# Kernel optimization log

Hardware: AMD Instinct MI355X
Metric: run time of the kernel (lower is better)

## Reference

```python
import jax, jax.numpy as jnp
import numpy as np

N_NODES = 100000
N_EDGES = 1600000
IN_FEATS = 256
DIMS = [IN_FEATS, 128, 64, 16, 40]


def setup_inputs() -> dict:
    key = jax.random.key(0)
    ks = jax.random.split(key, 3 + 2 * 4)
    x = jax.random.normal(ks[0], (N_NODES, IN_FEATS), dtype=jnp.float32)
    src = jax.random.randint(ks[1], (N_EDGES,), 0, N_NODES)
    dst = jax.random.randint(ks[2], (N_EDGES,), 0, N_NODES)
    inp = {"x": x, "src": src, "dst": dst}
    for i in range(4):
        fan_in = DIMS[i]
        inp[f"W{i+1}"] = jax.random.normal(ks[3 + 2 * i], (DIMS[i], DIMS[i + 1]), dtype=jnp.float32) / np.sqrt(fan_in)
        inp[f"b{i+1}"] = jnp.zeros((DIMS[i + 1],), dtype=jnp.float32)
    return inp


def reference(x, src, dst, W1, b1, W2, b2, W3, b3, W4, b4):
    n = x.shape[0]
    ones = jnp.ones(src.shape[0], dtype=x.dtype)
    # symmetric GCN normalization (DGL norm='both'); clamp deg>=1 like DGL
    deg_out = jnp.maximum(jax.ops.segment_sum(ones, src, num_segments=n), 1.0)
    deg_in = jnp.maximum(jax.ops.segment_sum(ones, dst, num_segments=n), 1.0)
    norm_src = jax.lax.rsqrt(deg_out)[:, None]  # [N,1]
    norm_dst = jax.lax.rsqrt(deg_in)[:, None]   # [N,1]

    def gconv(h, W, b, act):
        # project first (in_feats >= out_feats for every layer, matching DGL ordering)
        h = (h * norm_src) @ W                                   # [N, d_out]
        h = jax.ops.segment_sum(h[src], dst, num_segments=n)      # SpMM aggregate
        h = h * norm_dst + b
        return jax.nn.relu(h) if act else h

    h = gconv(x, W1, b1, True)
    h = gconv(h, W2, b2, True)
    h = gconv(h, W3, b3, True)
    h = gconv(h, W4, b4, False)
    return h
```

## Files before the change

kernel.cpp:

```cpp
#include <hip/hip_runtime.h>


typedef unsigned short ushort_t;
#define CAP 64

__device__ __forceinline__ void gload_lds16(const float4* g, float4* l) {
    __builtin_amdgcn_global_load_lds(
        (const __attribute__((address_space(1))) void*)g,
        (__attribute__((address_space(3))) void*)l, 16, 0, 0);
}

__device__ __forceinline__ ushort_t f2bf(float f) {
    unsigned u = __float_as_uint(f);
    u += 0x7FFFu + ((u >> 16) & 1u);
    return (ushort_t)(u >> 16);
}
__device__ __forceinline__ unsigned pack2bf(float a, float b) {
    return (unsigned)f2bf(a) | ((unsigned)f2bf(b) << 16);
}
__device__ __forceinline__ float nrm_of(int d) {
    return rsqrtf((float)(d > 1 ? d : 1));
}
#define BFLO(u) __uint_as_float((u) << 16)
#define BFHI(u) __uint_as_float((u) & 0xffff0000u)

template<int DIN, int DOUT, int RB, int KT, typename EPI>
__device__ __forceinline__ void proj_body(
        const float* __restrict__ in, const float* __restrict__ W,
        int N, int n0, float4* __restrict__ wlds, float4* __restrict__ xlds,
        EPI&& epi) {
    constexpr int CG  = DOUT / 4;
    constexpr int RPP = 256 / CG;
    constexpr int R4  = RB / RPP;
    constexpr int K4T = KT / 4;
    constexpr int NKT = DIN / KT;
    constexpr int XTILE = RB * K4T;
    constexpr int WTILE = KT * CG;

    const int tid  = threadIdx.x;
    const int wave = tid >> 6;
    const int lane = tid & 63;
    const int rp   = tid / CG;
    const int cg   = tid - rp * CG;

    float4 acc[R4];
#pragma unroll
    for (int r = 0; r < R4; ++r) acc[r] = make_float4(0.f, 0.f, 0.f, 0.f);

    for (int kt = 0; kt < NKT; ++kt) {
        const float4* wsrc = (const float4*)(W + (size_t)kt * KT * DOUT);
#pragma unroll
        for (int j = 0; j < WTILE / 256; ++j) {
            int base = j * 256 + wave * 64;
            gload_lds16(wsrc + base + lane, &wlds[base]);
        }
#pragma unroll
        for (int j = 0; j < XTILE / 256; ++j) {
            int base = j * 256 + wave * 64;
            int fi   = base + lane;
            int row  = fi / K4T;
            int k4   = fi - row * K4T;
            int k4s  = k4 ^ (row & (K4T - 1));
            int grow = n0 + row; if (grow >= N) grow = N - 1;
            const float4* gsrc = (const float4*)(in + (size_t)grow * DIN) + kt * K4T + k4s;
            gload_lds16(gsrc, &xlds[base]);
        }
        __syncthreads();
#pragma unroll 2
        for (int k4 = 0; k4 < K4T; ++k4) {
            float4 w0 = wlds[(k4 * 4 + 0) * CG + cg];
            float4 w1 = wlds[(k4 * 4 + 1) * CG + cg];
            float4 w2 = wlds[(k4 * 4 + 2) * CG + cg];
            float4 w3 = wlds[(k4 * 4 + 3) * CG + cg];
#pragma unroll
            for (int r = 0; r < R4; ++r) {
                int row = rp + r * RPP;
                float4 xv = xlds[row * K4T + (k4 ^ (row & (K4T - 1)))];
                acc[r].x = fmaf(xv.x, w0.x, acc[r].x);
                acc[r].y = fmaf(xv.x, w0.y, acc[r].y);
                acc[r].z = fmaf(xv.x, w0.z, acc[r].z);
                acc[r].w = fmaf(xv.x, w0.w, acc[r].w);
                acc[r].x = fmaf(xv.y, w1.x, acc[r].x);
                acc[r].y = fmaf(xv.y, w1.y, acc[r].y);
                acc[r].z = fmaf(xv.y, w1.z, acc[r].z);
                acc[r].w = fmaf(xv.y, w1.w, acc[r].w);
                acc[r].x = fmaf(xv.z, w2.x, acc[r].x);
                acc[r].y = fmaf(xv.z, w2.y, acc[r].y);
                acc[r].z = fmaf(xv.z, w2.z, acc[r].z);
                acc[r].w = fmaf(xv.z, w2.w, acc[r].w);
                acc[r].x = fmaf(xv.w, w3.x, acc[r].x);
                acc[r].y = fmaf(xv.w, w3.y, acc[r].y);
                acc[r].z = fmaf(xv.w, w3.z, acc[r].z);
                acc[r].w = fmaf(xv.w, w3.w, acc[r].w);
            }
        }
        __syncthreads();
    }
    epi(acc, rp, cg);
}

__device__ __forceinline__ void gather_l1_body(
        int n, int cb, const int* __restrict__ colp, const int* __restrict__ degO,
        const int* __restrict__ degI, const ushort_t* __restrict__ projbf,
        const float* __restrict__ bias, ushort_t* __restrict__ outbf) {
    constexpr int DOUT = 128;
    const int* cl = colp + (size_t)n * CAP;
    int dgi = degI[n];
    int dg = dgi > CAP ? CAP : dgi;
    float acc[8];
#pragma unroll
    for (int k = 0; k < 8; ++k) acc[k] = 0.f;
    int i = 0;
    for (; i + 4 <= dg; i += 4) {
        int4 ss = *(const int4*)(cl + i);
        uint4 v0 = *(const uint4*)(projbf + (size_t)ss.x * DOUT + cb * 8);
        uint4 v1 = *(const uint4*)(projbf + (size_t)ss.y * DOUT + cb * 8);
        uint4 v2 = *(const uint4*)(projbf + (size_t)ss.z * DOUT + cb * 8);
        uint4 v3 = *(const uint4*)(projbf + (size_t)ss.w * DOUT + cb * 8);
        float n0 = nrm_of(degO[ss.x]), n1 = nrm_of(degO[ss.y]);
        float n2 = nrm_of(degO[ss.z]), n3 = nrm_of(degO[ss.w]);
        acc[0] = fmaf(n0, BFLO(v0.x), fmaf(n1, BFLO(v1.x), fmaf(n2, BFLO(v2.x), fmaf(n3, BFLO(v3.x), acc[0]))));
        acc[1] = fmaf(n0, BFHI(v0.x), fmaf(n1, BFHI(v1.x), fmaf(n2, BFHI(v2.x), fmaf(n3, BFHI(v3.x), acc[1]))));
        acc[2] = fmaf(n0, BFLO(v0.y), fmaf(n1, BFLO(v1.y), fmaf(n2, BFLO(v2.y), fmaf(n3, BFLO(v3.y), acc[2]))));
        acc[3] = fmaf(n0, BFHI(v0.y), fmaf(n1, BFHI(v1.y), fmaf(n2, BFHI(v2.y), fmaf(n3, BFHI(v3.y), acc[3]))));
        acc[4] = fmaf(n0, BFLO(v0.z), fmaf(n1, BFLO(v1.z), fmaf(n2, BFLO(v2.z), fmaf(n3, BFLO(v3.z), acc[4]))));
        acc[5] = fmaf(n0, BFHI(v0.z), fmaf(n1, BFHI(v1.z), fmaf(n2, BFHI(v2.z), fmaf(n3, BFHI(v3.z), acc[5]))));
        acc[6] = fmaf(n0, BFLO(v0.w), fmaf(n1, BFLO(v1.w), fmaf(n2, BFLO(v2.w), fmaf(n3, BFLO(v3.w), acc[6]))));
        acc[7] = fmaf(n0, BFHI(v0.w), fmaf(n1, BFHI(v1.w), fmaf(n2, BFHI(v2.w), fmaf(n3, BFHI(v3.w), acc[7]))));
    }
    for (; i < dg; ++i) {
        int s0 = cl[i];
        uint4 v0 = *(const uint4*)(projbf + (size_t)s0 * DOUT + cb * 8);
        float ns0 = nrm_of(degO[s0]);
        acc[0] = fmaf(ns0, BFLO(v0.x), acc[0]);
        acc[1] = fmaf(ns0, BFHI(v0.x), acc[1]);
        acc[2] = fmaf(ns0, BFLO(v0.y), acc[2]);
        acc[3] = fmaf(ns0, BFHI(v0.y), acc[3]);
        acc[4] = fmaf(ns0, BFLO(v0.z), acc[4]);
        acc[5] = fmaf(ns0, BFHI(v0.z), acc[5]);
        acc[6] = fmaf(ns0, BFLO(v0.w), acc[6]);
        acc[7] = fmaf(ns0, BFHI(v0.w), acc[7]);
    }
    float nm = nrm_of(dgi);
    const float* bp = bias + cb * 8;
    float o[8];
#pragma unroll
    for (int k = 0; k < 8; ++k) o[k] = fmaxf(fmaf(acc[k], nm, bp[k]), 0.f);
    uint4 s;
    s.x = pack2bf(o[0], o[1]); s.y = pack2bf(o[2], o[3]);
    s.z = pack2bf(o[4], o[5]); s.w = pack2bf(o[6], o[7]);
    *(uint4*)(outbf + (size_t)n * DOUT + cb * 8) = s;
}

template<int DIN, int DOUT, int RB, int KT>
__global__ void __launch_bounds__(256) k_combA(
        const float* __restrict__ x, const float* __restrict__ W,
        ushort_t* __restrict__ outbf, int N,
        const int* __restrict__ src, const int* __restrict__ dst,
        int* __restrict__ degO, int* __restrict__ degI,
        int* __restrict__ colp, int E, int PB, int HTH, int NSPLIT) {
    constexpr int CG  = DOUT / 4;
    constexpr int RPP = 256 / CG;
    constexpr int R4  = RB / RPP;
    constexpr int K4T = KT / 4;
    __shared__ float4 wlds[KT * CG];
    __shared__ float4 xlds[RB * K4T];

    int bid = blockIdx.x, g = bid / 5, r = bid - g * 5;
    if (r == 4) {
        int i = g * 256 + (int)threadIdx.x;
        for (; i < E; i += HTH) {
            int s = src[i];
            int d = dst[i];
            atomicAdd(&degO[s], 1);
            if (d < NSPLIT) {
                int rk = atomicAdd(&degI[d], 1);
                if (rk < CAP) colp[(size_t)d * CAP + rk] = s;
            }
        }
        return;
    }
    int pidx = g * 4 + r;
    if (pidx >= PB) return;
    int n0 = pidx * RB;
    proj_body<DIN, DOUT, RB, KT>(x, W, N, n0, wlds, xlds,
        [&](float4 (&acc)[R4], int rp, int cg) {
#pragma unroll
            for (int rr = 0; rr < R4; ++rr) {
                int n = n0 + rp + rr * RPP;
                if (n < N) {
                    ushort4 s;
                    s.x = f2bf(acc[rr].x); s.y = f2bf(acc[rr].y);
                    s.z = f2bf(acc[rr].z); s.w = f2bf(acc[rr].w);
                    *(ushort4*)(outbf + (size_t)n * DOUT + cg * 4) = s;
                }
            }
        });
}

__global__ void __launch_bounds__(256) k_combB(
        const int* __restrict__ src, const int* __restrict__ dst,
        int* __restrict__ degI, int* __restrict__ colp,
        const int* __restrict__ degO, const ushort_t* __restrict__ projbf,
        const float* __restrict__ b1, ushort_t* __restrict__ h1bf,
        int NSPLIT, int E, int HTH) {
    int bid = blockIdx.x, g = bid / 5, r = bid - g * 5;
    if (r == 4) {
        int i = g * 256 + (int)threadIdx.x;
        for (; i < E; i += HTH) {
            int d = dst[i];
            if (d >= NSPLIT) {
                int rk = atomicAdd(&degI[d], 1);
                if (rk < CAP) colp[(size_t)d * CAP + rk] = src[i];
            }
        }
        return;
    }
    long t = ((long)(g * 4 + r)) * 256 + threadIdx.x;
    if (t >= (long)NSPLIT * 16) return;
    int n  = (int)(t >> 4);
    int cb = (int)(t & 15);
    gather_l1_body(n, cb, colp, degO, degI, projbf, b1, h1bf);
}

__global__ void __launch_bounds__(256) k_gather_l1(
        const int* __restrict__ colp, const int* __restrict__ degO,
        const int* __restrict__ degI, const ushort_t* __restrict__ projbf,
        const float* __restrict__ bias, ushort_t* __restrict__ outbf,
        int nlo, int N) {
    long t = blockIdx.x * 256L + threadIdx.x;
    if (t >= (long)(N - nlo) * 16) return;
    int n  = nlo + (int)(t >> 4);
    int cb = (int)(t & 15);
    gather_l1_body(n, cb, colp, degO, degI, projbf, bias, outbf);
}

__global__ void __launch_bounds__(256) k_proj_l2bf(
        const ushort_t* __restrict__ in, const int* __restrict__ degO,
        const float* __restrict__ W, ushort_t* __restrict__ outbf, int N) {
    __shared__ float4 wlds[32 * 16];
    __shared__ uint4  xlds[64 * 4];
    const int tid = threadIdx.x;
    const int rp = tid >> 4, cg = tid & 15;
    int n0 = blockIdx.x * 64;

    float4 acc[4];
#pragma unroll
    for (int r = 0; r < 4; ++r) acc[r] = make_float4(0.f, 0.f, 0.f, 0.f);

    for (int kt = 0; kt < 4; ++kt) {
        const float4* wsrc = (const float4*)(W + (size_t)kt * 32 * 64);
        gload_lds16(wsrc + tid, &wlds[tid]);
        gload_lds16(wsrc + 256 + tid, &wlds[256 + tid]);
        {
            int row = tid >> 2, c = tid & 3;
            int cs = c ^ (row & 3);
            int grow = n0 + row; if (grow >= N) grow = N - 1;
            const uint4* gsrc = (const uint4*)(in + (size_t)grow * 128) + kt * 4 + cs;
            gload_lds16((const float4*)gsrc, (float4*)&xlds[tid]);
        }
        __syncthreads();
#pragma unroll
        for (int k8 = 0; k8 < 4; ++k8) {
            float4 w[8];
#pragma unroll
            for (int j = 0; j < 8; ++j) w[j] = wlds[(k8 * 8 + j) * 16 + cg];
#pragma unroll
            for (int r = 0; r < 4; ++r) {
                int row = rp + r * 16;
                uint4 xv = xlds[row * 4 + (k8 ^ (row & 3))];
                float xf[8] = { BFLO(xv.x), BFHI(xv.x), BFLO(xv.y), BFHI(xv.y),
                                BFLO(xv.z), BFHI(xv.z), BFLO(xv.w), BFHI(xv.w) };
#pragma unroll
                for (int j = 0; j < 8; ++j) {
                    acc[r].x = fmaf(xf[j], w[j].x, acc[r].x);
                    acc[r].y = fmaf(xf[j], w[j].y, acc[r].y);
                    acc[r].z = fmaf(xf[j], w[j].z, acc[r].z);
                    acc[r].w = fmaf(xf[j], w[j].w, acc[r].w);
                }
            }
        }
        __syncthreads();
    }
#pragma unroll
    for (int r = 0; r < 4; ++r) {
        int n = n0 + rp + r * 16;
        if (n < N) {
            float nm = nrm_of(degO[n]);
            ushort4 s;
            s.x = f2bf(acc[r].x * nm); s.y = f2bf(acc[r].y * nm);
            s.z = f2bf(acc[r].z * nm); s.w = f2bf(acc[r].w * nm);
            *(ushort4*)(outbf + (size_t)n * 64 + cg * 4) = s;
        }
    }
}

__global__ void __launch_bounds__(256) k_gather_fuse2(
        const int* __restrict__ colp, const int* __restrict__ degO,
        const int* __restrict__ degI, const ushort_t* __restrict__ p2bf,
        const float* __restrict__ b2, const float* __restrict__ W3,
        float* __restrict__ P3, int N) {
    constexpr int DOUT = 64;
    __shared__ float w3s[64 * 16];
    ((float4*)w3s)[threadIdx.x] = ((const float4*)W3)[threadIdx.x];
    __syncthreads();

    long t = blockIdx.x * 256L + threadIdx.x;
    int n = (int)(t >> 3);
    bool valid = n < N;
    if (!valid) n = N - 1;
    int cb = (int)(t & 7);
    int lane = threadIdx.x & 63;
    int gb = lane & ~7;

    const int* cl = colp + (size_t)n * CAP;
    int dgi = degI[n];
    int dg = dgi > CAP ? CAP : dgi;
    float acc[8];
#pragma unroll
    for (int k = 0; k < 8; ++k) acc[k] = 0.f;
    int i = 0;
    for (; i + 4 <= dg; i += 4) {
        int4 ss = *(const int4*)(cl + i);
        uint4 v0 = *(const uint4*)(p2bf + (size_t)ss.x * DOUT + cb * 8);
        uint4 v1 = *(const uint4*)(p2bf + (size_t)ss.y * DOUT + cb * 8);
        uint4 v2 = *(const uint4*)(p2bf + (size_t)ss.z * DOUT + cb * 8);
        uint4 v3 = *(const uint4*)(p2bf + (size_t)ss.w * DOUT + cb * 8);
        acc[0] += BFLO(v0.x) + BFLO(v1.x) + BFLO(v2.x) + BFLO(v3.x);
        acc[1] += BFHI(v0.x) + BFHI(v1.x) + BFHI(v2.x) + BFHI(v3.x);
        acc[2] += BFLO(v0.y) + BFLO(v1.y) + BFLO(v2.y) + BFLO(v3.y);
        acc[3] += BFHI(v0.y) + BFHI(v1.y) + BFHI(v2.y) + BFHI(v3.y);
        acc[4] += BFLO(v0.z) + BFLO(v1.z) + BFLO(v2.z) + BFLO(v3.z);
        acc[5] += BFHI(v0.z) + BFHI(v1.z) + BFHI(v2.z) + BFHI(v3.z);
        acc[6] += BFLO(v0.w) + BFLO(v1.w) + BFLO(v2.w) + BFLO(v3.w);
        acc[7] += BFHI(v0.w) + BFHI(v1.w) + BFHI(v2.w) + BFHI(v3.w);
    }
    for (; i < dg; ++i) {
        int s0 = cl[i];
        uint4 v0 = *(const uint4*)(p2bf + (size_t)s0 * DOUT + cb * 8);
        acc[0] += BFLO(v0.x); acc[1] += BFHI(v0.x);
        acc[2] += BFLO(v0.y); acc[3] += BFHI(v0.y);
        acc[4] += BFLO(v0.z); acc[5] += BFHI(v0.z);
        acc[6] += BFLO(v0.w); acc[7] += BFHI(v0.w);
    }
    float nm = nrm_of(dgi);
    float ns = nrm_of(degO[n]);
    const float* bp = b2 + cb * 8;
    float o[8];
#pragma unroll
    for (int k = 0; k < 8; ++k)
        o[k] = fmaxf(fmaf(acc[k], nm, bp[k]), 0.f) * ns;
    float y0 = 0.f, y1 = 0.f;
#pragma unroll
    for (int k = 0; k < 64; ++k) {
        float v = __shfl(o[k & 7], gb + (k >> 3), 64);
        y0 = fmaf(v, w3s[k * 16 + 2 * cb], y0);
        y1 = fmaf(v, w3s[k * 16 + 2 * cb + 1], y1);
    }
    if (valid) *(float2*)(P3 + (size_t)n * 16 + 2 * cb) = make_float2(y0, y1);
}

__global__ void __launch_bounds__(256) k_gather_l3(
        const int* __restrict__ colp, const int* __restrict__ degO,
        const int* __restrict__ degI, const float* __restrict__ proj,
        const float* __restrict__ bias, float* __restrict__ out, int N) {
    long t = blockIdx.x * 256L + threadIdx.x;
    if (t >= (long)N * 4) return;
    int n  = (int)(t >> 2);
    int cg = (int)(t & 3);
    const int* cl = colp + (size_t)n * CAP;
    int dgi = degI[n];
    int dg = dgi > CAP ? CAP : dgi;
    float4 a0 = make_float4(0.f, 0.f, 0.f, 0.f);
    float4 a1 = make_float4(0.f, 0.f, 0.f, 0.f);
    float4 a2 = make_float4(0.f, 0.f, 0.f, 0.f);
    float4 a3 = make_float4(0.f, 0.f, 0.f, 0.f);
    int i = 0;
    for (; i + 4 <= dg; i += 4) {
        int4 ss = *(const int4*)(cl + i);
        float4 v0 = *(const float4*)(proj + (size_t)ss.x * 16 + cg * 4);
        float4 v1 = *(const float4*)(proj + (size_t)ss.y * 16 + cg * 4);
        float4 v2 = *(const float4*)(proj + (size_t)ss.z * 16 + cg * 4);
        float4 v3 = *(const float4*)(proj + (size_t)ss.w * 16 + cg * 4);
        a0.x += v0.x; a0.y += v0.y; a0.z += v0.z; a0.w += v0.w;
        a1.x += v1.x; a1.y += v1.y; a1.z += v1.z; a1.w += v1.w;
        a2.x += v2.x; a2.y += v2.y; a2.z += v2.z; a2.w += v2.w;
        a3.x += v3.x; a3.y += v3.y; a3.z += v3.z; a3.w += v3.w;
    }
    for (; i < dg; ++i) {
        int s0 = cl[i];
        float4 v0 = *(const float4*)(proj + (size_t)s0 * 16 + cg * 4);
        a0.x += v0.x; a0.y += v0.y; a0.z += v0.z; a0.w += v0.w;
    }
    float4 s = make_float4(a0.x + a1.x + a2.x + a3.x, a0.y + a1.y + a2.y + a3.y,
                           a0.z + a1.z + a2.z + a3.z, a0.w + a1.w + a2.w + a3.w);
    float nm = nrm_of(dgi);
    float ns = nrm_of(degO[n]);
    float4 b = *(const float4*)(bias + cg * 4);
    float4 o;
    o.x = fmaxf(fmaf(s.x, nm, b.x), 0.f) * ns;
    o.y = fmaxf(fmaf(s.y, nm, b.y), 0.f) * ns;
    o.z = fmaxf(fmaf(s.z, nm, b.z), 0.f) * ns;
    o.w = fmaxf(fmaf(s.w, nm, b.w), 0.f) * ns;
    *(float4*)(out + (size_t)n * 16 + cg * 4) = o;
}

__global__ void __launch_bounds__(256) k_gather_fuse4(
        const int* __restrict__ colp, const int* __restrict__ degI,
        const float* __restrict__ t4, const float* __restrict__ W4,
        const float* __restrict__ b4, float* __restrict__ out, int N) {
    __shared__ float w4s[16 * 40];
    __shared__ float b4s[40];
    for (int i = threadIdx.x; i < 160; i += 256)
        ((float4*)w4s)[i] = ((const float4*)W4)[i];
    if (threadIdx.x < 40) b4s[threadIdx.x] = b4[threadIdx.x];
    __syncthreads();

    long t = blockIdx.x * 256L + threadIdx.x;
    int n = (int)(t >> 2);
    bool valid = n < N;
    if (!valid) n = N - 1;
    int cg = (int)(t & 3);
    int lane = threadIdx.x & 63;
    int gb = lane & ~3;

    const int* cl = colp + (size_t)n * CAP;
    int dgi = degI[n];
    int dg = dgi > CAP ? CAP : dgi;
    float4 a0 = make_float4(0.f, 0.f, 0.f, 0.f);
    float4 a1 = make_float4(0.f, 0.f, 0.f, 0.f);
    int i = 0;
    for (; i + 2 <= dg; i += 2) {
        int2 ss = *(const int2*)(cl + i);
        float4 v0 = *(const float4*)(t4 + (size_t)ss.x * 16 + cg * 4);
        float4 v1 = *(const float4*)(t4 + (size_t)ss.y * 16 + cg * 4);
        a0.x += v0.x; a0.y += v0.y; a0.z += v0.z; a0.w += v0.w;
        a1.x += v1.x; a1.y += v1.y; a1.z += v1.z; a1.w += v1.w;
    }
    if (i < dg) {
        int s0 = cl[i];
        float4 v0 = *(const float4*)(t4 + (size_t)s0 * 16 + cg * 4);
        a0.x += v0.x; a0.y += v0.y; a0.z += v0.z; a0.w += v0.w;
    }
    float av[4] = { a0.x + a1.x, a0.y + a1.y, a0.z + a1.z, a0.w + a1.w };

    float y[10];
#pragma unroll
    for (int jj = 0; jj < 10; ++jj) y[jj] = 0.f;
#pragma unroll
    for (int k = 0; k < 16; ++k) {
        float v = __shfl(av[k & 3], gb + (k >> 2), 64);
        const float* wr = w4s + k * 40 + cg * 10;
#pragma unroll
        for (int jj = 0; jj < 10; ++jj) y[jj] = fmaf(v, wr[jj], y[jj]);
    }
    if (valid) {
        float nm = nrm_of(dgi);
        float* dp = out + (size_t)n * 40 + cg * 10;
        const float* bp = b4s + cg * 10;
#pragma unroll
        for (int jj = 0; jj < 10; ++jj) dp[jj] = fmaf(y[jj], nm, bp[jj]);
    }
}

static inline int cdiv(long a, int b) { return (int)((a + b - 1) / b); }

extern "C" void kernel_launch(void* const* d_in, const int* in_sizes, int n_in,
                              void* d_out, int out_size, void* d_ws, size_t ws_size,
                              hipStream_t stream) {
    const float* x   = (const float*)d_in[0];
    const int*   src = (const int*)d_in[1];
    const int*   dst = (const int*)d_in[2];
    const float* W1 = (const float*)d_in[3];  const float* b1 = (const float*)d_in[4];
    const float* W2 = (const float*)d_in[5];  const float* b2 = (const float*)d_in[6];
    const float* W3 = (const float*)d_in[7];  const float* b3 = (const float*)d_in[8];
    const float* W4 = (const float*)d_in[9];  const float* b4 = (const float*)d_in[10];

    const int N = in_sizes[0] / 256;
    const int E = in_sizes[1];
    const int NSPLIT = ((int)(0.65 * N) + 63) / 64 * 64;

    int* ws_i = (int*)d_ws;
    int* degO   = ws_i;
    int* degI   = ws_i + N;
    int* colp   = ws_i + 2 * (size_t)N;
    float* projb = (float*)(ws_i + 2 * (size_t)N + (size_t)N * CAP);
    float* hbuf  = projb + (size_t)N * 64;
    ushort_t* projbf = (ushort_t*)projb;
    ushort_t* h1bf   = (ushort_t*)hbuf;
    float* P3 = projb + (size_t)N * 32;

    int PB  = cdiv(N, 64);
    int G5A = cdiv(PB, 4);
    int HTHA = G5A * 256;

    long tB = (long)NSPLIT * 16;
    int G5B = cdiv(cdiv(tB, 256), 4);
    int HTHB = G5B * 256;

    hipMemsetAsync(degO, 0, 2 * (size_t)N * sizeof(int), stream);
    k_combA<256, 128, 64, 32><<<5 * G5A, 256, 0, stream>>>(
        x, W1, projbf, N, src, dst, degO, degI, colp, E, PB, HTHA, NSPLIT);

    k_combB<<<5 * G5B, 256, 0, stream>>>(
        src, dst, degI, colp, degO, projbf, b1, h1bf, NSPLIT, E, HTHB);

    k_gather_l1<<<cdiv((long)(N - NSPLIT) * 16, 256), 256, 0, stream>>>(
        colp, degO, degI, projbf, b1, h1bf, NSPLIT, N);

    k_proj_l2bf<<<cdiv(N, 64), 256, 0, stream>>>(h1bf, degO, W2, projbf, N);
    k_gather_fuse2<<<cdiv((long)N * 8, 256), 256, 0, stream>>>(
        colp, degO, degI, projbf, b2, W3, P3, N);

    k_gather_l3<<<cdiv((long)N * 4, 256), 256, 0, stream>>>(
        colp, degO, degI, P3, b3, hbuf, N);

    k_gather_fuse4<<<cdiv((long)N * 4, 256), 256, 0, stream>>>(
        colp, degI, hbuf, W4, b4, (float*)d_out, N);
}
```

Before: 348.0 us.

## Fuse layer-1 aggregation with layer-2 projection via wave shuffles

The layer-1 gather now applies bias and ReLU, then multiplies the 128-wide hidden row by W2 (staged in 32KB LDS per block) using cross-lane shuffles within 16-lane groups. This removes the separate layer-2 projection kernel and the round trip of h1 through global memory. The node split between the combined kernel and the tail kernel also moves from 65% to 50%. The cost is a 32KB LDS W2 copy per block, which lowers occupancy, plus 128 shuffles and LDS reads per thread for every node.

Result: faster. 333.1 us, median of 2 (-4.3%).

```diff
diff --git a/kernel.cpp b/kernel.cpp
--- a/kernel.cpp
+++ b/kernel.cpp
@@ -14,9 +14,6 @@
     unsigned u = __float_as_uint(f);
     u += 0x7FFFu + ((u >> 16) & 1u);
     return (ushort_t)(u >> 16);
-}
-__device__ __forceinline__ unsigned pack2bf(float a, float b) {
-    return (unsigned)f2bf(a) | ((unsigned)f2bf(b) << 16);
 }
 __device__ __forceinline__ float nrm_of(int d) {
     return rsqrtf((float)(d > 1 ? d : 1));
@@ -99,10 +96,11 @@
     epi(acc, rp, cg);
 }
 
-__device__ __forceinline__ void gather_l1_body(
-        int n, int cb, const int* __restrict__ colp, const int* __restrict__ degO,
-        const int* __restrict__ degI, const ushort_t* __restrict__ projbf,
-        const float* __restrict__ bias, ushort_t* __restrict__ outbf) {
+__device__ __forceinline__ void gl1p2_body(
+        int n, int cb, int gb, const int* __restrict__ colp,
+        const int* __restrict__ degO, const int* __restrict__ degI,
+        const ushort_t* __restrict__ p1bf, const float* __restrict__ b1,
+        const float* __restrict__ w2s, ushort_t* __restrict__ p2bf) {
     constexpr int DOUT = 128;
     const int* cl = colp + (size_t)n * CAP;
     int dgi = degI[n];
@@ -113,10 +111,10 @@
     int i = 0;
     for (; i + 4 <= dg; i += 4) {
         int4 ss = *(const int4*)(cl + i);
-        uint4 v0 = *(const uint4*)(projbf + (size_t)ss.x * DOUT + cb * 8);
-        uint4 v1 = *(const uint4*)(projbf + (size_t)ss.y * DOUT + cb * 8);
-        uint4 v2 = *(const uint4*)(projbf + (size_t)ss.z * DOUT + cb * 8);
-        uint4 v3 = *(const uint4*)(projbf + (size_t)ss.w * DOUT + cb * 8);
+        uint4 v0 = *(const uint4*)(p1bf + (size_t)ss.x * DOUT + cb * 8);
+        uint4 v1 = *(const uint4*)(p1bf + (size_t)ss.y * DOUT + cb * 8);
+        uint4 v2 = *(const uint4*)(p1bf + (size_t)ss.z * DOUT + cb * 8);
+        uint4 v3 = *(const uint4*)(p1bf + (size_t)ss.w * DOUT + cb * 8);
         float n0 = nrm_of(degO[ss.x]), n1 = nrm_of(degO[ss.y]);
         float n2 = nrm_of(degO[ss.z]), n3 = nrm_of(degO[ss.w]);
         acc[0] = fmaf(n0, BFLO(v0.x), fmaf(n1, BFLO(v1.x), fmaf(n2, BFLO(v2.x), fmaf(n3, BFLO(v3.x), acc[0]))));
@@ -130,7 +128,7 @@
     }
     for (; i < dg; ++i) {
         int s0 = cl[i];
-        uint4 v0 = *(const uint4*)(projbf + (size_t)s0 * DOUT + cb * 8);
+        uint4 v0 = *(const uint4*)(p1bf + (size_t)s0 * DOUT + cb * 8);
         float ns0 = nrm_of(degO[s0]);
         acc[0] = fmaf(ns0, BFLO(v0.x), acc[0]);
         acc[1] = fmaf(ns0, BFHI(v0.x), acc[1]);
@@ -142,14 +140,28 @@
         acc[7] = fmaf(ns0, BFHI(v0.w), acc[7]);
     }
     float nm = nrm_of(dgi);
-    const float* bp = bias + cb * 8;
+    const float* bp = b1 + cb * 8;
     float o[8];
 #pragma unroll
     for (int k = 0; k < 8; ++k) o[k] = fmaxf(fmaf(acc[k], nm, bp[k]), 0.f);
-    uint4 s;
-    s.x = pack2bf(o[0], o[1]); s.y = pack2bf(o[2], o[3]);
-    s.z = pack2bf(o[4], o[5]); s.w = pack2bf(o[6], o[7]);
-    *(uint4*)(outbf + (size_t)n * DOUT + cb * 8) = s;
+
+    float y0 = 0.f, y1 = 0.f, y2 = 0.f, y3 = 0.f;
+    for (int k8 = 0; k8 < 16; ++k8) {
+#pragma unroll
+        for (int j = 0; j < 8; ++j) {
+            float v = __shfl(o[j], gb + k8, 64);
+            const float4 w = *(const float4*)(w2s + (k8 * 8 + j) * 64 + cb * 4);
+            y0 = fmaf(v, w.x, y0);
+            y1 = fmaf(v, w.y, y1);
+            y2 = fmaf(v, w.z, y2);
+            y3 = fmaf(v, w.w, y3);
+        }
+    }
+    float ns = nrm_of(degO[n]);
+    ushort4 s;
+    s.x = f2bf(y0 * ns); s.y = f2bf(y1 * ns);
+    s.z = f2bf(y2 * ns); s.w = f2bf(y3 * ns);
+    *(ushort4*)(p2bf + (size_t)n * 64 + cb * 4) = s;
 }
 
 template<int DIN, int DOUT, int RB, int KT>
@@ -201,9 +213,10 @@
 __global__ void __launch_bounds__(256) k_combB(
         const int* __restrict__ src, const int* __restrict__ dst,
         int* __restrict__ degI, int* __restrict__ colp,
-        const int* __restrict__ degO, const ushort_t* __restrict__ projbf,
-        const float* __restrict__ b1, ushort_t* __restrict__ h1bf,
-        int NSPLIT, int E, int HTH) {
+        const int* __restrict__ degO, const ushort_t* __restrict__ p1bf,
+        const float* __restrict__ b1, const float* __restrict__ W2,
+        ushort_t* __restrict__ p2bf, int NSPLIT, int E, int HTH) {
+    __shared__ float w2s[128 * 64];
     int bid = blockIdx.x, g = bid / 5, r = bid - g * 5;
     if (r == 4) {
         int i = g * 256 + (int)threadIdx.x;
@@ -216,83 +229,36 @@
         }
         return;
     }
+#pragma unroll
+    for (int j = 0; j < 8; ++j)
+        gload_lds16((const float4*)W2 + j * 256 + threadIdx.x,
+                    (float4*)w2s + j * 256 + threadIdx.x);
+    __syncthreads();
     long t = ((long)(g * 4 + r)) * 256 + threadIdx.x;
     if (t >= (long)NSPLIT * 16) return;
     int n  = (int)(t >> 4);
     int cb = (int)(t & 15);
-    gather_l1_body(n, cb, colp, degO, degI, projbf, b1, h1bf);
-}
-
-__global__ void __launch_bounds__(256) k_gather_l1(
+    int gb = (threadIdx.x & 63) & ~15;
+    gl1p2_body(n, cb, gb, colp, degO, degI, p1bf, b1, w2s, p2bf);
+}
+
+__global__ void __launch_bounds__(256) k_gl1p2(
         const int* __restrict__ colp, const int* __restrict__ degO,
-        const int* __restrict__ degI, const ushort_t* __restrict__ projbf,
-        const float* __restrict__ bias, ushort_t* __restrict__ outbf,
-        int nlo, int N) {
+        const int* __restrict__ degI, const ushort_t* __restrict__ p1bf,
+        const float* __restrict__ b1, const float* __restrict__ W2,
+        ushort_t* __restrict__ p2bf, int nlo, int N) {
+    __shared__ float w2s[128 * 64];
+#pragma unroll
+    for (int j = 0; j < 8; ++j)
+        gload_lds16((const float4*)W2 + j * 256 + threadIdx.x,
+                    (float4*)w2s + j * 256 + threadIdx.x);
+    __syncthreads();
     long t = blockIdx.x * 256L + threadIdx.x;
     if (t >= (long)(N - nlo) * 16) return;
     int n  = nlo + (int)(t >> 4);
     int cb = (int)(t & 15);
-    gather_l1_body(n, cb, colp, degO, degI, projbf, bias, outbf);
-}
-
-__global__ void __launch_bounds__(256) k_proj_l2bf(
-        const ushort_t* __restrict__ in, const int* __restrict__ degO,
-        const float* __restrict__ W, ushort_t* __restrict__ outbf, int N) {
-    __shared__ float4 wlds[32 * 16];
-    __shared__ uint4  xlds[64 * 4];
-    const int tid = threadIdx.x;
-    const int rp = tid >> 4, cg = tid & 15;
-    int n0 = blockIdx.x * 64;
-
-    float4 acc[4];
-#pragma unroll
-    for (int r = 0; r < 4; ++r) acc[r] = make_float4(0.f, 0.f, 0.f, 0.f);
-
-    for (int kt = 0; kt < 4; ++kt) {
-        const float4* wsrc = (const float4*)(W + (size_t)kt * 32 * 64);
-        gload_lds16(wsrc + tid, &wlds[tid]);
-        gload_lds16(wsrc + 256 + tid, &wlds[256 + tid]);
-        {
-            int row = tid >> 2, c = tid & 3;
-            int cs = c ^ (row & 3);
-            int grow = n0 + row; if (grow >= N) grow = N - 1;
-            const uint4* gsrc = (const uint4*)(in + (size_t)grow * 128) + kt * 4 + cs;
-            gload_lds16((const float4*)gsrc, (float4*)&xlds[tid]);
-        }
-        __syncthreads();
-#pragma unroll
-        for (int k8 = 0; k8 < 4; ++k8) {
-            float4 w[8];
-#pragma unroll
-            for (int j = 0; j < 8; ++j) w[j] = wlds[(k8 * 8 + j) * 16 + cg];
-#pragma unroll
-            for (int r = 0; r < 4; ++r) {
-                int row = rp + r * 16;
-                uint4 xv = xlds[row * 4 + (k8 ^ (row & 3))];
-                float xf[8] = { BFLO(xv.x), BFHI(xv.x), BFLO(xv.y), BFHI(xv.y),
-                                BFLO(xv.z), BFHI(xv.z), BFLO(xv.w), BFHI(xv.w) };
-#pragma unroll
-                for (int j = 0; j < 8; ++j) {
-                    acc[r].x = fmaf(xf[j], w[j].x, acc[r].x);
-                    acc[r].y = fmaf(xf[j], w[j].y, acc[r].y);
-                    acc[r].z = fmaf(xf[j], w[j].z, acc[r].z);
-                    acc[r].w = fmaf(xf[j], w[j].w, acc[r].w);
-                }
-            }
-        }
-        __syncthreads();
-    }
-#pragma unroll
-    for (int r = 0; r < 4; ++r) {
-        int n = n0 + rp + r * 16;
-        if (n < N) {
-            float nm = nrm_of(degO[n]);
-            ushort4 s;
-            s.x = f2bf(acc[r].x * nm); s.y = f2bf(acc[r].y * nm);
-            s.z = f2bf(acc[r].z * nm); s.w = f2bf(acc[r].w * nm);
-            *(ushort4*)(outbf + (size_t)n * 64 + cg * 4) = s;
-        }
-    }
+    int gb = (threadIdx.x & 63) & ~15;
+    gl1p2_body(n, cb, gb, colp, degO, degI, p1bf, b1, w2s, p2bf);
 }
 
 __global__ void __launch_bounds__(256) k_gather_fuse2(
@@ -478,17 +444,17 @@
 
     const int N = in_sizes[0] / 256;
     const int E = in_sizes[1];
-    const int NSPLIT = ((int)(0.65 * N) + 63) / 64 * 64;
+    const int NSPLIT = ((N / 2) + 63) / 64 * 64;
 
     int* ws_i = (int*)d_ws;
     int* degO   = ws_i;
     int* degI   = ws_i + N;
     int* colp   = ws_i + 2 * (size_t)N;
-    float* projb = (float*)(ws_i + 2 * (size_t)N + (size_t)N * CAP);
-    float* hbuf  = projb + (size_t)N * 64;
-    ushort_t* projbf = (ushort_t*)projb;
-    ushort_t* h1bf   = (ushort_t*)hbuf;
-    float* P3 = projb + (size_t)N * 32;
+    float* fbase = (float*)(ws_i + 2 * (size_t)N + (size_t)N * CAP);
+    ushort_t* p1bf = (ushort_t*)fbase;
+    ushort_t* p2bf = (ushort_t*)(fbase + (size_t)N * 64);
+    float* P3 = fbase + (size_t)N * 96;
+    float* t4 = fbase + (size_t)N * 112;
 
     int PB  = cdiv(N, 64);
     int G5A = cdiv(PB, 4);
@@ -500,21 +466,20 @@
 
     hipMemsetAsync(degO, 0, 2 * (size_t)N * sizeof(int), stream);
     k_combA<256, 128, 64, 32><<<5 * G5A, 256, 0, stream>>>(
-        x, W1, projbf, N, src, dst, degO, degI, colp, E, PB, HTHA, NSPLIT);
+        x, W1, p1bf, N, src, dst, degO, degI, colp, E, PB, HTHA, NSPLIT);
 
     k_combB<<<5 * G5B, 256, 0, stream>>>(
-        src, dst, degI, colp, degO, projbf, b1, h1bf, NSPLIT, E, HTHB);
-
-    k_gather_l1<<<cdiv((long)(N - NSPLIT) * 16, 256), 256, 0, stream>>>(
-        colp, degO, degI, projbf, b1, h1bf, NSPLIT, N);
-
-    k_proj_l2bf<<<cdiv(N, 64), 256, 0, stream>>>(h1bf, degO, W2, projbf, N);
+        src, dst, degI, colp, degO, p1bf, b1, W2, p2bf, NSPLIT, E, HTHB);
+
+    k_gl1p2<<<cdiv((long)(N - NSPLIT) * 16, 256), 256, 0, stream>>>(
+        colp, degO, degI, p1bf, b1, W2, p2bf, NSPLIT, N);
+
     k_gather_fuse2<<<cdiv((long)N * 8, 256), 256, 0, stream>>>(
-        colp, degO, degI, projbf, b2, W3, P3, N);
+        colp, degO, degI, p2bf, b2, W3, P3, N);
 
     k_gather_l3<<<cdiv((long)N * 4, 256), 256, 0, stream>>>(
-        colp, degO, degI, P3, b3, hbuf, N);
+        colp, degO, degI, P3, b3, t4, N);
 
     k_gather_fuse4<<<cdiv((long)N * 4, 256), 256, 0, stream>>>(
-        colp, degI, hbuf, W4, b4, (float*)d_out, N);
-}
+        colp, degI, t4, W4, b4, (float*)d_out, N);
+}
```
